# Kernel optimization log

Hardware: AMD Instinct MI355X
Metric: run time of the kernel (lower is better)

Reference implementation:

```python
import jax, jax.numpy as jnp
import numpy as np

B, C, L, D = 8, 32, 2048, 128
R, H = 8, 4  # num_routers, num_heads


def setup_inputs() -> dict:
    key = jax.random.key(0)
    ks = jax.random.split(key, 20)
    p = lambda k, shape: jax.random.normal(k, shape, dtype=jnp.float32) * 0.02
    inp = {
        "Z": jax.random.normal(ks[0], (B, C, L, D), dtype=jnp.float32),
        "router": p(ks[1], (R, D)),
        # router_sender projections (d_model -> d_model, torch Linear stored as x@W+b)
        "Wq1": p(ks[2], (D, D)), "bq1": jnp.zeros((D,), jnp.float32),
        "Wk1": p(ks[3], (D, D)), "bk1": jnp.zeros((D,), jnp.float32),
        "Wv1": p(ks[4], (D, D)), "bv1": jnp.zeros((D,), jnp.float32),
        "Wo1": p(ks[5], (D, D)), "bo1": jnp.zeros((D,), jnp.float32),
        # router_receiver projections
        "Wq2": p(ks[6], (D, D)), "bq2": jnp.zeros((D,), jnp.float32),
        "Wk2": p(ks[7], (D, D)), "bk2": jnp.zeros((D,), jnp.float32),
        "Wv2": p(ks[8], (D, D)), "bv2": jnp.zeros((D,), jnp.float32),
        "Wo2": p(ks[9], (D, D)), "bo2": jnp.zeros((D,), jnp.float32),
        # LayerNorm
        "gamma": jnp.ones((D,), jnp.float32),
        "beta": jnp.zeros((D,), jnp.float32),
    }
    return inp


def _cross_attn(q_in, k_in, v_in, Wq, bq, Wk, bk, Wv, bv, Wo, bo):
    # Informer FullAttention + AttentionLayer (dropout=0)
    Bn, Lq, Dm = q_in.shape
    Lk = k_in.shape[1]
    dh = Dm // H
    q = (q_in @ Wq + bq).reshape(Bn, Lq, H, dh)
    k = (k_in @ Wk + bk).reshape(Bn, Lk, H, dh)
    v = (v_in @ Wv + bv).reshape(Bn, Lk, H, dh)
    scale = 1.0 / np.sqrt(dh)
    scores = jnp.einsum("blhe,bshe->bhls", q, k) * scale
    A = jax.nn.softmax(scores, axis=-1)
    out = jnp.einsum("bhls,bshd->blhd", A, v).reshape(Bn, Lq, Dm)
    return out @ Wo + bo


def _layernorm(x, gamma, beta, eps=1e-5):
    mu = jnp.mean(x, axis=-1, keepdims=True)
    var = jnp.mean(jnp.square(x - mu), axis=-1, keepdims=True)
    return (x - mu) * jax.lax.rsqrt(var + eps) * gamma + beta


def reference(Z, router, Wq1, bq1, Wk1, bk1, Wv1, bv1, Wo1, bo1,
              Wq2, bq2, Wk2, bk2, Wv2, bv2, Wo2, bo2, gamma, beta):
    Bz, Cz, Lz, Dz = Z.shape
    x = Z.reshape(Bz * Cz, Lz, Dz)
    batch_router = jnp.broadcast_to(router[None], (Bz * Cz, R, Dz))
    # stage 1: routers attend to the sequence (R x L)
    router_buffer = _cross_attn(batch_router, x, x,
                                Wq1, bq1, Wk1, bk1, Wv1, bv1, Wo1, bo1)
    # stage 2: sequence attends to routers (L x R)
    router_receive = _cross_attn(x, router_buffer, router_buffer,
                                 Wq2, bq2, Wk2, bk2, Wv2, bv2, Wo2, bo2)
    out = _layernorm(x + router_receive, gamma, beta)
    return out.reshape(Bz, Cz, Lz, Dz)
```

## Files before the change

kernel.cpp:

```cpp
#include <hip/hip_runtime.h>

typedef float f4_t __attribute__((ext_vector_type(4)));
typedef __bf16 bf8_t __attribute__((ext_vector_type(8)));
typedef __bf16 bf4_t __attribute__((ext_vector_type(4)));

#define MFMA16(a,b,c) __builtin_amdgcn_mfma_f32_16x16x32_bf16((a),(b),(c),0,0,0)

static constexpr float kScale = 0.17677669529663687f;

__device__ __forceinline__ void bar_lds() {
  asm volatile("s_waitcnt lgkmcnt(0)" ::: "memory");
  __builtin_amdgcn_s_barrier();
}

__global__ __launch_bounds__(256) void k0_fold(
    const float* __restrict__ router, const float* __restrict__ Wq1,
    const float* __restrict__ bq1, const float* __restrict__ Wk1,
    const float* __restrict__ bk1, __bf16* __restrict__ q1t,
    float* __restrict__ c1)
{
  __shared__ float q1[8][128];
  const int t = threadIdx.x, b = blockIdx.x;
  for (int idx = t; idx < 1024; idx += 256) {
    int r = idx >> 7, dp = idx & 127;
    float acc = bq1[dp];
    for (int e = 0; e < 128; ++e) acc += router[r*128 + e] * Wq1[e*128 + dp];
    q1[r][dp] = acc;
  }
  __syncthreads();
  {
    int idx = b*256 + t;
    int j = idx >> 7, e = idx & 127;
    int h = j >> 3, r = j & 7;
    float acc = 0.f;
    for (int d = 0; d < 32; ++d) acc += q1[r][h*32 + d] * Wk1[e*128 + h*32 + d];
    q1t[idx] = (__bf16)(acc * kScale);
  }
  if (b == 0 && t < 32) {
    int h = t >> 3, r = t & 7;
    float acc = 0.f;
    for (int d = 0; d < 32; ++d) acc += q1[r][h*32 + d] * bk1[h*32 + d];
    c1[t] = acc * kScale;
  }
}

__global__ __launch_bounds__(512) void k1_stage1(
    const float* __restrict__ Z, const __bf16* __restrict__ q1t_g,
    const float* __restrict__ c1_g, float* __restrict__ xap,
    float* __restrict__ lp, __bf16* __restrict__ xws)
{
  __shared__ __bf16 xb[64][136];
  __shared__ __bf16 xT[128][72];
  __shared__ __bf16 PT[32][72];
  __shared__ float lds_l[32];

  const int tid = threadIdx.x;
  const int bid = blockIdx.x;
  const float* xbase = Z + (size_t)bid * (256 * 128);
  __bf16* xwb = xws + (size_t)bid * (256 * 128);

  if (tid < 32) lds_l[tid] = 0.f;

  const int lane = tid & 63;
  const int w = tid >> 6;
  const int lc = lane & 15;
  const int lg = lane >> 4;
  const int ms = w >> 2;
  const int ns = w & 3;
  float c1v[4];
#pragma unroll
  for (int r2 = 0; r2 < 4; ++r2) c1v[r2] = c1_g[ms*16 + lg*4 + r2];
  bf8_t aq[4];
#pragma unroll
  for (int ks = 0; ks < 4; ++ks)
    aq[ks] = *(const bf8_t*)(q1t_g + (ms*16 + lc)*128 + ks*32 + lg*8);

  const f4_t fzero = {0.f, 0.f, 0.f, 0.f};
  f4_t accxa[2] = { fzero, fzero };
  float Lacc[4] = {0.f, 0.f, 0.f, 0.f};

  const int srow = tid >> 4;
  const int sd0  = (tid & 15) << 3;

  f4_t zr[4];
#pragma unroll
  for (int i = 0; i < 2; ++i) {
    const float* p = xbase + (srow + 32*i)*128 + sd0;
    zr[i*2]   = __builtin_nontemporal_load((const f4_t*)p);
    zr[i*2+1] = __builtin_nontemporal_load((const f4_t*)(p + 4));
  }

  bar_lds();

  for (int tile = 0; tile < 4; ++tile) {
#pragma unroll
    for (int i = 0; i < 2; ++i) {
      int pos = srow + 32*i;
      f4_t v0 = zr[i*2], v1 = zr[i*2+1];
      bf8_t b8 = { (__bf16)v0.x, (__bf16)v0.y, (__bf16)v0.z, (__bf16)v0.w,
                   (__bf16)v1.x, (__bf16)v1.y, (__bf16)v1.z, (__bf16)v1.w };
      *(bf8_t*)&xb[pos][sd0] = b8;
      *(bf8_t*)(xwb + (tile*64 + pos)*128 + sd0) = b8;
    }
    bar_lds();

    if (tile < 3) {
      const float* xt = xbase + (tile + 1) * (64 * 128);
#pragma unroll
      for (int i = 0; i < 2; ++i) {
        const float* p = xt + (srow + 32*i)*128 + sd0;
        zr[i*2]   = __builtin_nontemporal_load((const f4_t*)p);
        zr[i*2+1] = __builtin_nontemporal_load((const f4_t*)(p + 4));
      }
    }

#pragma unroll
    for (int s = 0; s < 2; ++s) {
      int u = tid + s*512;
      int dim = u & 127, pb = (u >> 7) << 3;
      bf8_t t8;
#pragma unroll
      for (int p = 0; p < 8; ++p) t8[p] = xb[pb + p][dim];
      *(bf8_t*)&xT[dim][pb] = t8;
    }
    f4_t sacc = fzero;
#pragma unroll
    for (int ks = 0; ks < 4; ++ks) {
      bf8_t b = *(const bf8_t*)&xb[ns*16 + lc][ks*32 + lg*8];
      sacc = MFMA16(aq[ks], b, sacc);
    }
    const int posn = ns*16 + lc;
#pragma unroll
    for (int r2 = 0; r2 < 4; ++r2) {
      float p = __expf(sacc[r2] + c1v[r2]);
      Lacc[r2] += p;
      PT[ms*16 + lg*4 + r2][posn] = (__bf16)p;
    }
    bar_lds();

#pragma unroll
    for (int nt = 0; nt < 2; ++nt) {
      const int dimt = (ns << 1) + nt;
#pragma unroll
      for (int ks = 0; ks < 2; ++ks) {
        bf8_t a = *(const bf8_t*)&xT[dimt*16 + lc][ks*32 + lg*8];
        bf8_t b = *(const bf8_t*)&PT[ms*16 + lc][ks*32 + lg*8];
        accxa[nt] = MFMA16(a, b, accxa[nt]);
      }
    }
  }

#pragma unroll
  for (int r2 = 0; r2 < 4; ++r2) {
    float v = Lacc[r2];
    v += __shfl_xor(v, 1);
    v += __shfl_xor(v, 2);
    v += __shfl_xor(v, 4);
    v += __shfl_xor(v, 8);
    if (lc == 0) atomicAdd(&lds_l[ms*16 + lg*4 + r2], v);
  }
  bar_lds();

  float* xo = xap + (size_t)bid * 4096;
  const int jrow = ms*16 + lc;
#pragma unroll
  for (int nt = 0; nt < 2; ++nt) {
    const int dim0 = ((ns << 1) + nt)*16 + lg*4;
    *(f4_t*)(xo + jrow*128 + dim0) = accxa[nt];
  }
  if (tid < 32) lp[bid*32 + tid] = lds_l[tid];
}

__global__ __launch_bounds__(256) void k1b_mid(
    const float* __restrict__ xap, const float* __restrict__ lp,
    const float* __restrict__ Wv1, const float* __restrict__ bv1,
    const float* __restrict__ Wo1, const float* __restrict__ bo1,
    const float* __restrict__ Wk2, const float* __restrict__ bk2,
    const float* __restrict__ Wv2, const float* __restrict__ bv2,
    const float* __restrict__ Wq2, const float* __restrict__ bq2,
    const float* __restrict__ Wo2,
    __bf16* __restrict__ kt2, float* __restrict__ c2, __bf16* __restrict__ vt2)
{
  __shared__ float xa[32][129];
  __shared__ float invl[32];
  __shared__ float out1[8][128];
  __shared__ float rb[8][128];
  __shared__ float k2s[8][128];
  __shared__ float v2s[8][128];

  const int t = threadIdx.x, b = blockIdx.x;
  for (int idx = t; idx < 4096; idx += 256) {
    float s = 0.f;
#pragma unroll
    for (int k = 0; k < 8; ++k)
      s += xap[(size_t)(b*8 + k) * 4096 + idx];
    xa[idx >> 7][idx & 127] = s;
  }
  if (t < 32) {
    float s = 0.f;
#pragma unroll
    for (int k = 0; k < 8; ++k) s += lp[(b*8 + k)*32 + t];
    invl[t] = 1.f / s;
  }
  bar_lds();

  for (int idx = t; idx < 1024; idx += 256) {
    int r = idx >> 7, hd = idx & 127, h = hd >> 5;
    int j = h*8 + r;
    float acc = 0.f;
    for (int e = 0; e < 128; ++e) acc += xa[j][e] * Wv1[e*128 + hd];
    out1[r][hd] = acc * invl[j] + bv1[hd];
  }
  bar_lds();
  for (int idx = t; idx < 1024; idx += 256) {
    int r = idx >> 7, e2 = idx & 127;
    float acc = bo1[e2];
    for (int hd = 0; hd < 128; ++hd) acc += out1[r][hd] * Wo1[hd*128 + e2];
    rb[r][e2] = acc;
  }
  bar_lds();
  for (int idx = t; idx < 2048; idx += 256) {
    int sel = idx >> 10;
    int r = (idx >> 7) & 7, hd = idx & 127;
    const float* W = sel ? Wv2 : Wk2;
    const float* bb = sel ? bv2 : bk2;
    float acc = bb[hd];
    for (int e = 0; e < 128; ++e) acc += rb[r][e] * W[e*128 + hd];
    float (*dst)[128] = sel ? v2s : k2s;
    dst[r][hd] = acc;
  }
  bar_lds();
  for (int idx = t; idx < 4096; idx += 256) {
    int j = idx >> 7, e = idx & 127;
    int h = j >> 3, r = j & 7;
    float acck = 0.f, accv = 0.f;
    for (int d = 0; d < 32; ++d) {
      acck += Wq2[e*128 + h*32 + d] * k2s[r][h*32 + d];
      accv += v2s[r][h*32 + d] * Wo2[(h*32 + d)*128 + e];
    }
    kt2[(size_t)b*4096 + j*128 + e] = (__bf16)(acck * kScale);
    vt2[(size_t)b*4096 + e*32 + j] = (__bf16)accv;
  }
  if (t < 32) {
    int h = t >> 3, r = t & 7;
    float acc = 0.f;
    for (int d = 0; d < 32; ++d) acc += bq2[h*32 + d] * k2s[r][h*32 + d];
    c2[b*32 + t] = acc * kScale;
  }
}

__global__ __launch_bounds__(512) void k2_stage2(
    const __bf16* __restrict__ xws, const __bf16* __restrict__ kt2,
    const float* __restrict__ c2g, const __bf16* __restrict__ vt2,
    const float* __restrict__ bo2, const float* __restrict__ gamma,
    const float* __restrict__ beta, float* __restrict__ out)
{
  __shared__ __bf16 xb[128][136];
  __shared__ __bf16 P2[128][40];

  const int tid = threadIdx.x;
  const int blk = blockIdx.x;
  const int batch = blk >> 1;

  const __bf16* ktb = kt2 + (size_t)batch * 4096;
  const __bf16* vtb = vt2 + (size_t)batch * 4096;

  const int lane = tid & 63;
  const int w = tid >> 6;
  const int lc = lane & 15;
  const int lg = lane >> 4;

  float c2v[2] = { c2g[batch*32 + lc], c2g[batch*32 + 16 + lc] };
  f4_t bo2v[8], gv[8], bv[8];
#pragma unroll
  for (int nt = 0; nt < 8; ++nt) {
    int dd = nt*16 + lg*4;
    bo2v[nt] = *(const f4_t*)(bo2 + dd);
    gv[nt]   = *(const f4_t*)(gamma + dd);
    bv[nt]   = *(const f4_t*)(beta + dd);
  }
  bf8_t vfrag[8];
#pragma unroll
  for (int nt = 0; nt < 8; ++nt)
    vfrag[nt] = *(const bf8_t*)(vtb + (nt*16 + lc)*32 + lg*8);

  int spos[4], sd[4];
#pragma unroll
  for (int j = 0; j < 4; ++j) {
    int c = lane + j*64;
    spos[j] = w*16 + (c >> 4);
    sd[j]   = (c & 15) << 3;
  }

  const size_t base0 = (size_t)blk * 8 * 16384;
  uint4 zx[4];
#pragma unroll
  for (int j = 0; j < 4; ++j)
    zx[j] = *(const uint4*)(xws + base0 + spos[j]*128 + sd[j]);

  const f4_t fzero = {0.f, 0.f, 0.f, 0.f};

  for (int c = 0; c < 8; ++c) {
    const size_t cb = base0 + (size_t)c * 16384;
#pragma unroll
    for (int j = 0; j < 4; ++j)
      *(uint4*)&xb[spos[j]][sd[j]] = zx[j];
    if (c < 7) {
#pragma unroll
      for (int j = 0; j < 4; ++j)
        zx[j] = *(const uint4*)(xws + cb + 16384 + spos[j]*128 + sd[j]);
    }

    f4_t sacc[2] = { fzero, fzero };
#pragma unroll
    for (int ks = 0; ks < 4; ++ks) {
      bf8_t a = *(const bf8_t*)&xb[w*16 + lc][ks*32 + lg*8];
#pragma unroll
      for (int nt = 0; nt < 2; ++nt) {
        bf8_t b = *(const bf8_t*)(ktb + (nt*16 + lc)*128 + ks*32 + lg*8);
        sacc[nt] = MFMA16(a, b, sacc[nt]);
      }
    }
#pragma unroll
    for (int nt = 0; nt < 2; ++nt) {
#pragma unroll
      for (int r2 = 0; r2 < 4; ++r2) {
        float p = __expf(sacc[nt][r2] + c2v[nt]);
        float sum = p;
        sum += __shfl_xor(sum, 1);
        sum += __shfl_xor(sum, 2);
        sum += __shfl_xor(sum, 4);
        P2[w*16 + lg*4 + r2][nt*16 + lc] = (__bf16)(p * __builtin_amdgcn_rcpf(sum));
      }
    }

    bf8_t pf = *(const bf8_t*)&P2[w*16 + lc][lg*8];
    f4_t racc[8];
#pragma unroll
    for (int nt = 0; nt < 8; ++nt)
      racc[nt] = MFMA16(vfrag[nt], pf, fzero);

    const int pos = w*16 + lc;
    float s1 = 0.f, s2 = 0.f;
#pragma unroll
    for (int nt = 0; nt < 8; ++nt) {
      bf4_t xq = *(const bf4_t*)&xb[pos][nt*16 + lg*4];
#pragma unroll
      for (int r = 0; r < 4; ++r) {
        float tv = racc[nt][r] + bo2v[nt][r] + (float)xq[r];
        racc[nt][r] = tv;
        s1 += tv; s2 += tv*tv;
      }
    }
    s1 += __shfl_xor(s1, 16); s1 += __shfl_xor(s1, 32);
    s2 += __shfl_xor(s2, 16); s2 += __shfl_xor(s2, 32);
    float mean = s1 * (1.f/128.f);
    float var = s2 * (1.f/128.f) - mean*mean;
    float rstd = rsqrtf(var + 1e-5f);

    float* y = out + cb + (size_t)pos*128;
#pragma unroll
    for (int nt = 0; nt < 8; ++nt) {
      f4_t o;
#pragma unroll
      for (int r = 0; r < 4; ++r)
        o[r] = (racc[nt][r] - mean) * rstd * gv[nt][r] + bv[nt][r];
      __builtin_nontemporal_store(o, (f4_t*)(y + nt*16 + lg*4));
    }
  }
}

extern "C" void kernel_launch(void* const* d_in, const int* in_sizes, int n_in,
                              void* d_out, int out_size, void* d_ws, size_t ws_size,
                              hipStream_t stream)
{
  const float* Z     = (const float*)d_in[0];
  const float* router= (const float*)d_in[1];
  const float* Wq1   = (const float*)d_in[2];
  const float* bq1   = (const float*)d_in[3];
  const float* Wk1   = (const float*)d_in[4];
  const float* bk1   = (const float*)d_in[5];
  const float* Wv1   = (const float*)d_in[6];
  const float* bv1   = (const float*)d_in[7];
  const float* Wo1   = (const float*)d_in[8];
  const float* bo1   = (const float*)d_in[9];
  const float* Wq2   = (const float*)d_in[10];
  const float* bq2   = (const float*)d_in[11];
  const float* Wk2   = (const float*)d_in[12];
  const float* bk2   = (const float*)d_in[13];
  const float* Wv2   = (const float*)d_in[14];
  const float* bv2   = (const float*)d_in[15];
  const float* Wo2   = (const float*)d_in[16];
  const float* bo2   = (const float*)d_in[17];
  const float* gamma = (const float*)d_in[18];
  const float* beta  = (const float*)d_in[19];
  float* out = (float*)d_out;

  char* base = (char*)d_ws;
  __bf16* q1tb = (__bf16*)(base);
  float*  c1   = (float*)(base + 8192);
  float*  c2   = (float*)(base + 16384);
  float*  lp   = (float*)(base + 65536);
  float*  xap  = (float*)(base + (1u<<20));
  __bf16* kt2b = (__bf16*)(base + (36u<<20));
  __bf16* vt2b = (__bf16*)(base + (38u<<20));
  __bf16* xws  = (__bf16*)(base + (40u<<20));
  (void)in_sizes; (void)n_in; (void)out_size; (void)ws_size;

  k0_fold<<<dim3(16), dim3(256), 0, stream>>>(router, Wq1, bq1, Wk1, bk1, q1tb, c1);
  k1_stage1<<<dim3(2048), dim3(512), 0, stream>>>(Z, q1tb, c1, xap, lp, xws);
  k1b_mid<<<dim3(256), dim3(256), 0, stream>>>(xap, lp, Wv1, bv1, Wo1, bo1,
                                               Wk2, bk2, Wv2, bv2, Wq2, bq2, Wo2,
                                               kt2b, c2, vt2b);
  k2_stage2<<<dim3(512), dim3(512), 0, stream>>>(xws, kt2b, c2, vt2b, bo2, gamma, beta, out);
}
```

Measured before the change: 294.0 us.

## Split stage-2 into small one-shot blocks reading x directly from global

Stage 2 used 512 persistent-style blocks of 512 threads, each looping over 8 chunks of 128 rows and staging them in LDS with register prefetch. It now launches 8192 blocks of 256 threads, each handling 64 rows once. The x tile is read straight from global memory for the MFMA A operand and the residual, and the xb LDS buffer is removed. This aims to raise occupancy and parallelism and to drop LDS staging. In exchange, each block reloads the per-batch K/V fragments and the bias, gamma and beta vectors, reads x twice from global, and loses the explicit prefetch overlap.

```diff
diff --git a/kernel.cpp b/kernel.cpp
--- a/kernel.cpp
+++ b/kernel.cpp
@@ -249,18 +249,19 @@
   }
 }
 
-__global__ __launch_bounds__(512) void k2_stage2(
+__global__ __launch_bounds__(256) void k2_stage2(
     const __bf16* __restrict__ xws, const __bf16* __restrict__ kt2,
     const float* __restrict__ c2g, const __bf16* __restrict__ vt2,
     const float* __restrict__ bo2, const float* __restrict__ gamma,
     const float* __restrict__ beta, float* __restrict__ out)
 {
-  __shared__ __bf16 xb[128][136];
-  __shared__ __bf16 P2[128][40];
+  __shared__ __bf16 P2[64][40];
 
   const int tid = threadIdx.x;
-  const int blk = blockIdx.x;
-  const int batch = blk >> 1;
+  const int bid = blockIdx.x;
+  const int batch = bid >> 5;
+  const __bf16* xsrc = xws + (size_t)bid * (64 * 128);
+  float* y = out + (size_t)bid * (64 * 128);
 
   const __bf16* ktb = kt2 + (size_t)batch * 4096;
   const __bf16* vtb = vt2 + (size_t)batch * 4096;
@@ -269,104 +270,70 @@
   const int w = tid >> 6;
   const int lc = lane & 15;
   const int lg = lane >> 4;
-
+  const int pos = w*16 + lc;
+
+  const f4_t fzero = {0.f, 0.f, 0.f, 0.f};
+
+  f4_t sacc[2] = { fzero, fzero };
+#pragma unroll
+  for (int ks = 0; ks < 4; ++ks) {
+    bf8_t a = *(const bf8_t*)(xsrc + pos*128 + ks*32 + lg*8);
+#pragma unroll
+    for (int nt = 0; nt < 2; ++nt) {
+      bf8_t b = *(const bf8_t*)(ktb + (nt*16 + lc)*128 + ks*32 + lg*8);
+      sacc[nt] = MFMA16(a, b, sacc[nt]);
+    }
+  }
   float c2v[2] = { c2g[batch*32 + lc], c2g[batch*32 + 16 + lc] };
-  f4_t bo2v[8], gv[8], bv[8];
+#pragma unroll
+  for (int nt = 0; nt < 2; ++nt) {
+#pragma unroll
+    for (int r2 = 0; r2 < 4; ++r2) {
+      float p = __expf(sacc[nt][r2] + c2v[nt]);
+      float sum = p;
+      sum += __shfl_xor(sum, 1);
+      sum += __shfl_xor(sum, 2);
+      sum += __shfl_xor(sum, 4);
+      P2[w*16 + lg*4 + r2][nt*16 + lc] = (__bf16)(p * __builtin_amdgcn_rcpf(sum));
+    }
+  }
+
+  bf8_t pf = *(const bf8_t*)&P2[w*16 + lc][lg*8];
+  f4_t racc[8];
 #pragma unroll
   for (int nt = 0; nt < 8; ++nt) {
-    int dd = nt*16 + lg*4;
-    bo2v[nt] = *(const f4_t*)(bo2 + dd);
-    gv[nt]   = *(const f4_t*)(gamma + dd);
-    bv[nt]   = *(const f4_t*)(beta + dd);
-  }
-  bf8_t vfrag[8];
-#pragma unroll
-  for (int nt = 0; nt < 8; ++nt)
-    vfrag[nt] = *(const bf8_t*)(vtb + (nt*16 + lc)*32 + lg*8);
-
-  int spos[4], sd[4];
-#pragma unroll
-  for (int j = 0; j < 4; ++j) {
-    int c = lane + j*64;
-    spos[j] = w*16 + (c >> 4);
-    sd[j]   = (c & 15) << 3;
-  }
-
-  const size_t base0 = (size_t)blk * 8 * 16384;
-  uint4 zx[4];
-#pragma unroll
-  for (int j = 0; j < 4; ++j)
-    zx[j] = *(const uint4*)(xws + base0 + spos[j]*128 + sd[j]);
-
-  const f4_t fzero = {0.f, 0.f, 0.f, 0.f};
-
-  for (int c = 0; c < 8; ++c) {
-    const size_t cb = base0 + (size_t)c * 16384;
-#pragma unroll
-    for (int j = 0; j < 4; ++j)
-      *(uint4*)&xb[spos[j]][sd[j]] = zx[j];
-    if (c < 7) {
-#pragma unroll
-      for (int j = 0; j < 4; ++j)
-        zx[j] = *(const uint4*)(xws + cb + 16384 + spos[j]*128 + sd[j]);
-    }
-
-    f4_t sacc[2] = { fzero, fzero };
-#pragma unroll
-    for (int ks = 0; ks < 4; ++ks) {
-      bf8_t a = *(const bf8_t*)&xb[w*16 + lc][ks*32 + lg*8];
-#pragma unroll
-      for (int nt = 0; nt < 2; ++nt) {
-        bf8_t b = *(const bf8_t*)(ktb + (nt*16 + lc)*128 + ks*32 + lg*8);
-        sacc[nt] = MFMA16(a, b, sacc[nt]);
-      }
-    }
-#pragma unroll
-    for (int nt = 0; nt < 2; ++nt) {
-#pragma unroll
-      for (int r2 = 0; r2 < 4; ++r2) {
-        float p = __expf(sacc[nt][r2] + c2v[nt]);
-        float sum = p;
-        sum += __shfl_xor(sum, 1);
-        sum += __shfl_xor(sum, 2);
-        sum += __shfl_xor(sum, 4);
-        P2[w*16 + lg*4 + r2][nt*16 + lc] = (__bf16)(p * __builtin_amdgcn_rcpf(sum));
-      }
-    }
-
-    bf8_t pf = *(const bf8_t*)&P2[w*16 + lc][lg*8];
-    f4_t racc[8];
-#pragma unroll
-    for (int nt = 0; nt < 8; ++nt)
-      racc[nt] = MFMA16(vfrag[nt], pf, fzero);
-
-    const int pos = w*16 + lc;
-    float s1 = 0.f, s2 = 0.f;
-#pragma unroll
-    for (int nt = 0; nt < 8; ++nt) {
-      bf4_t xq = *(const bf4_t*)&xb[pos][nt*16 + lg*4];
-#pragma unroll
-      for (int r = 0; r < 4; ++r) {
-        float tv = racc[nt][r] + bo2v[nt][r] + (float)xq[r];
-        racc[nt][r] = tv;
-        s1 += tv; s2 += tv*tv;
-      }
-    }
-    s1 += __shfl_xor(s1, 16); s1 += __shfl_xor(s1, 32);
-    s2 += __shfl_xor(s2, 16); s2 += __shfl_xor(s2, 32);
-    float mean = s1 * (1.f/128.f);
-    float var = s2 * (1.f/128.f) - mean*mean;
-    float rstd = rsqrtf(var + 1e-5f);
-
-    float* y = out + cb + (size_t)pos*128;
-#pragma unroll
-    for (int nt = 0; nt < 8; ++nt) {
-      f4_t o;
-#pragma unroll
-      for (int r = 0; r < 4; ++r)
-        o[r] = (racc[nt][r] - mean) * rstd * gv[nt][r] + bv[nt][r];
-      __builtin_nontemporal_store(o, (f4_t*)(y + nt*16 + lg*4));
-    }
+    bf8_t vfr = *(const bf8_t*)(vtb + (nt*16 + lc)*32 + lg*8);
+    racc[nt] = MFMA16(vfr, pf, fzero);
+  }
+
+  float s1 = 0.f, s2 = 0.f;
+#pragma unroll
+  for (int nt = 0; nt < 8; ++nt) {
+    bf4_t xq = *(const bf4_t*)(xsrc + pos*128 + nt*16 + lg*4);
+    f4_t bq = *(const f4_t*)(bo2 + nt*16 + lg*4);
+#pragma unroll
+    for (int r = 0; r < 4; ++r) {
+      float tv = racc[nt][r] + bq[r] + (float)xq[r];
+      racc[nt][r] = tv;
+      s1 += tv; s2 += tv*tv;
+    }
+  }
+  s1 += __shfl_xor(s1, 16); s1 += __shfl_xor(s1, 32);
+  s2 += __shfl_xor(s2, 16); s2 += __shfl_xor(s2, 32);
+  float mean = s1 * (1.f/128.f);
+  float var = s2 * (1.f/128.f) - mean*mean;
+  float rstd = rsqrtf(var + 1e-5f);
+
+  float* yp = y + (size_t)pos*128;
+#pragma unroll
+  for (int nt = 0; nt < 8; ++nt) {
+    f4_t gq = *(const f4_t*)(gamma + nt*16 + lg*4);
+    f4_t bb = *(const f4_t*)(beta + nt*16 + lg*4);
+    f4_t o;
+#pragma unroll
+    for (int r = 0; r < 4; ++r)
+      o[r] = (racc[nt][r] - mean) * rstd * gq[r] + bb[r];
+    __builtin_nontemporal_store(o, (f4_t*)(yp + nt*16 + lg*4));
   }
 }
 
@@ -412,5 +379,5 @@
   k1b_mid<<<dim3(256), dim3(256), 0, stream>>>(xap, lp, Wv1, bv1, Wo1, bo1,
                                                Wk2, bk2, Wv2, bv2, Wq2, bq2, Wo2,
                                                kt2b, c2, vt2b);
-  k2_stage2<<<dim3(512), dim3(512), 0, stream>>>(xws, kt2b, c2, vt2b, bo2, gamma, beta, out);
-}
+  k2_stage2<<<dim3(8192), dim3(256), 0, stream>>>(xws, kt2b, c2, vt2b, bo2, gamma, beta, out);
+}
```

New measurement: 328.4 us. +11.7%, slower.
